# Performance work log

Hardware: AMD Instinct MI355X
Metric: run time of the kernel (lower is better)

The kernel has to match this reference:

```python
import jax, jax.numpy as jnp
import numpy as np

ALPHA = 0.3          # triplet margin
LOSS_WEIGHT = 1.0
VALID_COST = 100.0   # chosen so all queries are valid (query2gt ~ U[0,1))
POS_T = 3            # pos_thresh
NEG_T = 30           # neg_thresh
EPS = 1e-6           # torch pairwise_distance eps


def setup_inputs() -> dict:
    key0 = jax.random.key(0)
    ks = jax.random.split(key0, 6)
    Nq, V, K, D, G = 2048, 6, 4096, 256, 64
    attn = jax.random.normal(ks[0], (Nq, V, K), dtype=jnp.float32)
    query2gt = jax.random.uniform(ks[1], (Nq, G), dtype=jnp.float32)  # min < VALID_COST always
    query = jax.random.normal(ks[2], (Nq, V, D), dtype=jnp.float32)
    key = jax.random.normal(ks[3], (K, V, D), dtype=jnp.float32)
    pos_idx = jax.random.randint(ks[4], (V * Nq,), 0, POS_T, dtype=jnp.int64 if jax.config.jax_enable_x64 else jnp.int32)
    neg_idx = jax.random.randint(ks[5], (V * Nq,), POS_T, NEG_T, dtype=jnp.int64 if jax.config.jax_enable_x64 else jnp.int32)
    return {"attn": attn, "query2gt": query2gt, "query": query, "key": key,
            "pos_idx": pos_idx, "neg_idx": neg_idx}


def reference(attn, query2gt, query, key, pos_idx, neg_idx):
    # valid filtering: query2gt.min(-1) < VALID_COST is all-True by construction,
    # so no rows are dropped (keeps shapes static under jit).
    q = jnp.transpose(query, (1, 0, 2))   # [V, Nq, D]
    k = jnp.transpose(key, (1, 0, 2))     # [V, K, D]
    a = jnp.transpose(attn, (1, 0, 2))    # [V, Nq, K]
    V, Nq, K = a.shape

    # batched euclidean cdist per view via gram expansion
    qq = jnp.sum(q * q, axis=-1)[:, :, None]          # [V, Nq, 1]
    kk = jnp.sum(k * k, axis=-1)[:, None, :]          # [V, 1, K]
    d2 = qq + kk - 2.0 * jnp.einsum('vnd,vkd->vnk', q, k)
    dist = jnp.sqrt(jnp.maximum(d2, 0.0))             # [V, Nq, K]

    sorted_idx = jnp.argsort(dist, axis=-1).reshape(V * Nq, K)
    a = a.reshape(V * Nq, K)
    r = jnp.arange(V * Nq)

    pos = jax.nn.sigmoid(a[r, sorted_idx[r, pos_idx]])  # [V*Nq]
    neg = jax.nn.sigmoid(a[r, sorted_idx[r, neg_idx]])  # [V*Nq]

    # TripletMarginLoss(margin=ALPHA, p=1) with anchor = ones, 1-d embeddings
    d_pos = jnp.abs(1.0 - pos + EPS)
    d_neg = jnp.abs(1.0 - neg + EPS)
    loss = jnp.mean(jnp.maximum(d_pos - d_neg + ALPHA, 0.0))
    return LOSS_WEIGHT * loss
```

## Files before the change

kernel.cpp:

```cpp
#include <hip/hip_runtime.h>
#include <stdint.h>

#define NQ    2048
#define VV    6
#define KCNT  4096
#define DD    256
#define NROWS (VV*NQ)
#define ALPHA_M 0.3f
#define EPSL  1e-6f
#define SBIAS 256.0f
#define ZTHR  2.05f
#define CAP   256
#define NCHUNK 64
#define SLOTS  16

#define TM 128
#define TN 128
#define BKK 32

typedef _Float16 f16x8 __attribute__((ext_vector_type(8)));
typedef _Float16 f16x4 __attribute__((ext_vector_type(4)));
typedef float    f32x4 __attribute__((ext_vector_type(4)));

__device__ __forceinline__ void gload16(const void* g, void* l) {
    __builtin_amdgcn_global_load_lds(
        (__attribute__((address_space(1))) void*)(uintptr_t)g,
        (__attribute__((address_space(3))) void*)(uintptr_t)(uint32_t)(uintptr_t)l,
        16, 0, 0);
}

__device__ __forceinline__ unsigned ord16(_Float16 h) {
    unsigned short b = __builtin_bit_cast(unsigned short, h);
    return (b & 0x8000u) ? (unsigned)(~b & 0xFFFFu) : (unsigned)(b | 0x8000u);
}

__device__ __forceinline__ float triplet_term(const float* attn, int r, int kpos, int kneg) {
    int v = r / NQ, q = r - v * NQ;
    float apos = attn[(size_t)q * (VV*KCNT) + v*KCNT + kpos];
    float aneg = attn[(size_t)q * (VV*KCNT) + v*KCNT + kneg];
    float pv = 1.0f / (1.0f + expf(-apos));
    float nv = 1.0f / (1.0f + expf(-aneg));
    float dp = fabsf(1.0f - pv + EPSL);
    float dn = fabsf(1.0f - nv + EPSL);
    return fmaxf(dp - dn + ALPHA_M, 0.0f);
}

__global__ __launch_bounds__(256) void pack_fused(const float* __restrict__ key,
                                                  const float* __restrict__ query,
                                                  _Float16* __restrict__ Bpack,
                                                  _Float16* __restrict__ Apack,
                                                  float* __restrict__ kkp,
                                                  float* __restrict__ Trow,
                                                  unsigned* __restrict__ fcount,
                                                  float* __restrict__ out)
{
    int wid  = threadIdx.x >> 6;
    int lane = threadIdx.x & 63;
    if (blockIdx.x < 6144) {
        int rowid = blockIdx.x * 4 + wid;
        int k = rowid / 6;
        int v = rowid - k * 6;
        float4 x = *(const float4*)(key + (size_t)rowid * DD + lane * 4);
        f16x4 h;
        h.x = (_Float16)x.x; h.y = (_Float16)x.y;
        h.z = (_Float16)x.z; h.w = (_Float16)x.w;
        *(f16x4*)(Bpack + ((size_t)(v * KCNT + k)) * DD + lane * 4) = h;

        float s = x.x*x.x + x.y*x.y + x.z*x.z + x.w*x.w;
        #pragma unroll
        for (int off = 32; off >= 1; off >>= 1) s += __shfl_xor(s, off);
        if (lane == 0) kkp[v * KCNT + k] = s;
    } else {
        int bid2 = blockIdx.x - 6144;
        if (bid2 == 0) {
            if (threadIdx.x == 0) *fcount = 0;
            if (threadIdx.x == 1) out[0] = 0.0f;
        }
        int rowid = bid2 * 4 + wid;
        int q = rowid / 6;
        int v = rowid - q * 6;
        float4 x = *(const float4*)(query + (size_t)rowid * DD + lane * 4);
        f16x4 h;
        h.x = (_Float16)x.x; h.y = (_Float16)x.y;
        h.z = (_Float16)x.z; h.w = (_Float16)x.w;
        *(f16x4*)(Apack + ((size_t)(v * NQ + q)) * DD + lane * 4) = h;

        float qq = x.x*x.x + x.y*x.y + x.z*x.z + x.w*x.w;
        #pragma unroll
        for (int off = 32; off >= 1; off >>= 1) qq += __shfl_xor(qq, off);
        if (lane == 0)
            Trow[v * NQ + q] = 256.0f - ZTHR * sqrtf(512.0f + 4.0f * qq);
    }
}

__global__ __launch_bounds__(256) void score_gemm(const _Float16* __restrict__ Apack,
                                                  const _Float16* __restrict__ Bpack,
                                                  const float* __restrict__ kkp,
                                                  const float* __restrict__ Trow,
                                                  unsigned* __restrict__ cnt2,
                                                  unsigned* __restrict__ cand)
{
    __shared__ _Float16 As[TM * BKK];
    __shared__ _Float16 Bs[TN * BKK];

    int tid  = threadIdx.x;
    int wid  = tid >> 6;
    int lane = tid & 63;
    int c0   = blockIdx.x * TN;
    int grow = blockIdx.y * TM;
    int v    = grow / NQ;
    int q0   = grow - v * NQ;

    int srow = (wid << 4) + (lane >> 2);
    int sseg = (lane & 3) ^ ((lane >> 2) & 3);
    const _Float16* Ag0 = Apack + ((size_t)(v*NQ   + q0 + srow)) * DD + sseg*8;
    const _Float16* Ag1 = Ag0 + (size_t)64 * DD;
    const _Float16* Bg0 = Bpack + ((size_t)(v*KCNT + c0 + srow)) * DD + sseg*8;
    const _Float16* Bg1 = Bg0 + (size_t)64 * DD;

    _Float16* lA0 = As + wid*512;
    _Float16* lA1 = As + 2048 + wid*512;
    _Float16* lB0 = Bs + wid*512;
    _Float16* lB1 = Bs + 2048 + wid*512;

    int fr = lane & 15;
    int kg = lane >> 4;
    int rb = (wid >> 1) * 64;
    int cb = (wid & 1) * 64;
    int rg = lane >> 4;
    int ksw = (kg ^ (fr & 3)) << 3;

    f32x4 acc[4][4] = {};

    for (int kb = 0; kb < DD; kb += BKK) {
        __syncthreads();
        gload16(Ag0 + kb, lA0);
        gload16(Ag1 + kb, lA1);
        gload16(Bg0 + kb, lB0);
        gload16(Bg1 + kb, lB1);
        __syncthreads();

        f16x8 af[4], bf[4];
        #pragma unroll
        for (int m = 0; m < 4; ++m)
            af[m] = *(const f16x8*)&As[(rb + m*16 + fr)*BKK + ksw];
        #pragma unroll
        for (int n = 0; n < 4; ++n)
            bf[n] = *(const f16x8*)&Bs[(cb + n*16 + fr)*BKK + ksw];
        #pragma unroll
        for (int m = 0; m < 4; ++m)
            #pragma unroll
            for (int n = 0; n < 4; ++n)
                acc[m][n] = __builtin_amdgcn_mfma_f32_16x16x32_f16(af[m], bf[n], acc[m][n], 0, 0, 0);
    }

    int chunk = blockIdx.x * 2 + (wid & 1);
    float kkv[4];
    #pragma unroll
    for (int n = 0; n < 4; ++n)
        kkv[n] = kkp[v*KCNT + c0 + cb + n*16 + fr];

    unsigned ltm = (1u << fr) - 1u;
    int sh = rg * 16;

    #pragma unroll
    for (int m = 0; m < 4; ++m) {
        #pragma unroll
        for (int j = 0; j < 4; ++j) {
            int gr = grow + rb + m*16 + rg*4 + j;
            float Tr = Trow[gr];
            float s[4];
            unsigned g16[4];
            #pragma unroll
            for (int n = 0; n < 4; ++n) {
                s[n] = kkv[n] - 2.0f * acc[m][n][j];
                unsigned long long bal = __ballot(s[n] < Tr);
                g16[n] = (unsigned)(bal >> sh) & 0xFFFFu;
            }
            unsigned rank = 0;
            #pragma unroll
            for (int n = 0; n < 4; ++n) {
                if (s[n] < Tr) {
                    unsigned pos = rank + __popc(g16[n] & ltm);
                    if (pos < SLOTS)
                        cand[((size_t)gr << 10) + (chunk << 4) + pos] =
                            (ord16((_Float16)(s[n] - SBIAS)) << 12)
                            | (unsigned)(c0 + cb + n*16 + fr);
                }
                rank += __popc(g16[n]);
            }
            if (fr == 0) cnt2[(gr << 6) + chunk] = rank;
        }
    }
}

__global__ __launch_bounds__(256) void select2_kernel(const unsigned* __restrict__ cnt2,
                                                      const unsigned* __restrict__ cand,
                                                      const float* __restrict__ attn,
                                                      const int* __restrict__ pos_idx,
                                                      const int* __restrict__ neg_idx,
                                                      unsigned* __restrict__ fcount,
                                                      int* __restrict__ flist,
                                                      float* __restrict__ out)
{
    __shared__ unsigned cbuf[4][CAP];
    __shared__ float bsum;
    if (threadIdx.x == 0) bsum = 0.0f;
    __syncthreads();

    int wid  = threadIdx.x >> 6;
    int lane = threadIdx.x & 63;
    int r    = blockIdx.x * 4 + wid;
    int p = pos_idx[r];
    int n = neg_idx[r];

    unsigned c_l = cnt2[(r << 6) + lane];
    unsigned pre = c_l;
    #pragma unroll
    for (int off = 1; off <= 32; off <<= 1) {
        unsigned o = __shfl_up(pre, off);
        if (lane >= off) pre += o;
    }
    unsigned total = __shfl(pre, 63);
    unsigned excl  = pre - c_l;
    bool overflow  = __any(c_l > SLOTS);

    if (overflow || total < (unsigned)(n + 1) || total > CAP) {
        if (lane == 0) {
            unsigned i = atomicAdd(fcount, 1u);
            flist[i] = r;
        }
    } else {
        unsigned* mybuf = cbuf[wid];
        const unsigned* src = cand + ((size_t)r << 10) + (lane << 4);
        for (unsigned i = 0; i < c_l; ++i) mybuf[excl + i] = src[i];
        __asm__ volatile("s_waitcnt lgkmcnt(0)" ::: "memory");

        unsigned v0 = (lane       < (int)total) ? mybuf[lane]       : 0xFFFFFFFFu;
        unsigned v1 = (lane + 64  < (int)total) ? mybuf[lane + 64]  : 0xFFFFFFFFu;
        unsigned v2 = (lane + 128 < (int)total) ? mybuf[lane + 128] : 0xFFFFFFFFu;
        unsigned v3 = (lane + 192 < (int)total) ? mybuf[lane + 192] : 0xFFFFFFFFu;
        int kpos = 0, kneg = 0;
        for (int t = 0; t <= n; ++t) {
            unsigned m01 = v0 < v1 ? v0 : v1;
            unsigned m23 = v2 < v3 ? v2 : v3;
            unsigned m = m01 < m23 ? m01 : m23;
            #pragma unroll
            for (int off = 32; off >= 1; off >>= 1) {
                unsigned o = __shfl_xor(m, off);
                m = o < m ? o : m;
            }
            if      (v0 == m) v0 = 0xFFFFFFFFu;
            else if (v1 == m) v1 = 0xFFFFFFFFu;
            else if (v2 == m) v2 = 0xFFFFFFFFu;
            else if (v3 == m) v3 = 0xFFFFFFFFu;
            if (t == p) kpos = (int)(m & 0xFFFu);
            if (t == n) kneg = (int)(m & 0xFFFu);
        }
        if (lane == 0)
            atomicAdd(&bsum, triplet_term(attn, r, kpos, kneg) * (1.0f / (float)NROWS));
    }
    __syncthreads();
    if (threadIdx.x == 0) atomicAdd(out, bsum);
}

__global__ __launch_bounds__(256) void fallback_kernel(const _Float16* __restrict__ Apack,
                                                       const _Float16* __restrict__ Bpack,
                                                       const float* __restrict__ kkp,
                                                       const float* __restrict__ attn,
                                                       const int* __restrict__ pos_idx,
                                                       const int* __restrict__ neg_idx,
                                                       const unsigned* __restrict__ fcount,
                                                       const int* __restrict__ flist,
                                                       float* __restrict__ out)
{
    __shared__ float qrow[DD];
    __shared__ unsigned keys[KCNT];
    int nf = (int)*fcount;
    for (int it = blockIdx.x; it < nf; it += gridDim.x) {
        int r = flist[it];
        int v = r / NQ, q = r - v * NQ;
        qrow[threadIdx.x] = (float)Apack[((size_t)(v*NQ + q)) * DD + threadIdx.x];
        __syncthreads();
        for (int i = 0; i < 16; ++i) {
            int c = i * 256 + threadIdx.x;
            float dot = 0.0f;
            const f16x8* bp = (const f16x8*)(Bpack + ((size_t)(v*KCNT + c)) * DD);
            for (int d8 = 0; d8 < 32; ++d8) {
                f16x8 b = bp[d8];
                #pragma unroll
                for (int j = 0; j < 8; ++j) dot += qrow[d8*8 + j] * (float)b[j];
            }
            float s = kkp[v*KCNT + c] - 2.0f * dot;
            keys[c] = (ord16((_Float16)(s - SBIAS)) << 12) | (unsigned)c;
        }
        __syncthreads();
        if (threadIdx.x < 64) {
            int lane = threadIdx.x;
            int p = pos_idx[r], n = neg_idx[r];
            unsigned prev = 0;
            int kpos = 0, kneg = 0;
            for (int t = 0; t <= n; ++t) {
                unsigned m = 0xFFFFFFFFu;
                for (int i = 0; i < 64; ++i) {
                    unsigned kk2 = keys[i*64 + lane];
                    if (kk2 > prev && kk2 < m) m = kk2;
                }
                #pragma unroll
                for (int off = 32; off >= 1; off >>= 1) {
                    unsigned o = __shfl_xor(m, off);
                    m = o < m ? o : m;
                }
                if (t == p) kpos = (int)(m & 0xFFFu);
                if (t == n) kneg = (int)(m & 0xFFFu);
                prev = m;
            }
            if (lane == 0)
                atomicAdd(out, triplet_term(attn, r, kpos, kneg) * (1.0f / (float)NROWS));
        }
        __syncthreads();
    }
}

extern "C" void kernel_launch(void* const* d_in, const int* in_sizes, int n_in,
                              void* d_out, int out_size, void* d_ws, size_t ws_size,
                              hipStream_t stream)
{
    const float* attn    = (const float*)d_in[0];
    const float* query   = (const float*)d_in[2];
    const float* key     = (const float*)d_in[3];
    const int*   pos_idx = (const int*)d_in[4];
    const int*   neg_idx = (const int*)d_in[5];
    float* out = (float*)d_out;

    char* w = (char*)d_ws;
    unsigned* fcount   = (unsigned*)(w);
    float*    Trow     = (float*)   (w + 256);
    float*    kkp      = (float*)   (w + 49408);
    unsigned* cnt2     = (unsigned*)(w + 147712);
    int*      flist    = (int*)     (w + 3293440);
    _Float16* Apack    = (_Float16*)(w + 3342592);
    _Float16* Bpack    = (_Float16*)(w + 9634048);
    unsigned* cand     = (unsigned*)(w + 22216960);

    pack_fused<<<9216, 256, 0, stream>>>(key, query, Bpack, Apack, kkp, Trow,
                                         fcount, out);

    dim3 gg(KCNT / TN, NROWS / TM);
    score_gemm<<<gg, 256, 0, stream>>>(Apack, Bpack, kkp, Trow, cnt2, cand);

    select2_kernel<<<NROWS / 4, 256, 0, stream>>>(cnt2, cand, attn, pos_idx, neg_idx,
                                                  fcount, flist, out);
    fallback_kernel<<<64, 256, 0, stream>>>(Apack, Bpack, kkp, attn, pos_idx, neg_idx,
                                            fcount, flist, out);
}
```

Baseline: 129.4 us.

## Replace compacted candidate slots with per-chunk bitmasks and dense fp16 score matrix

The score GEMM no longer compacts threshold-passing candidates into fixed 16-slot buckets with counts. It now writes every score as fp16 into a dense row-major matrix, plus a 64-bit ballot mask per 64-column chunk. The select kernel popcounts the masks to build prefix offsets, then gathers the selected scores through the set bits. This removes the per-chunk slot-overflow fallback path and the rank computation in the GEMM epilogue, but adds a full fp16 write of the whole score matrix and scattered 2-byte gathers in the select kernel.

```diff
diff --git a/kernel.cpp b/kernel.cpp
--- a/kernel.cpp
+++ b/kernel.cpp
@@ -11,8 +11,6 @@
 #define SBIAS 256.0f
 #define ZTHR  2.05f
 #define CAP   256
-#define NCHUNK 64
-#define SLOTS  16
 
 #define TM 128
 #define TN 128
@@ -97,8 +95,8 @@
                                                   const _Float16* __restrict__ Bpack,
                                                   const float* __restrict__ kkp,
                                                   const float* __restrict__ Trow,
-                                                  unsigned* __restrict__ cnt2,
-                                                  unsigned* __restrict__ cand)
+                                                  unsigned long long* __restrict__ maskb,
+                                                  _Float16* __restrict__ wsf)
 {
     __shared__ _Float16 As[TM * BKK];
     __shared__ _Float16 Bs[TN * BKK];
@@ -160,7 +158,6 @@
     for (int n = 0; n < 4; ++n)
         kkv[n] = kkp[v*KCNT + c0 + cb + n*16 + fr];
 
-    unsigned ltm = (1u << fr) - 1u;
     int sh = rg * 16;
 
     #pragma unroll
@@ -169,33 +166,21 @@
         for (int j = 0; j < 4; ++j) {
             int gr = grow + rb + m*16 + rg*4 + j;
             float Tr = Trow[gr];
-            float s[4];
-            unsigned g16[4];
+            unsigned long long mk = 0;
             #pragma unroll
             for (int n = 0; n < 4; ++n) {
-                s[n] = kkv[n] - 2.0f * acc[m][n][j];
-                unsigned long long bal = __ballot(s[n] < Tr);
-                g16[n] = (unsigned)(bal >> sh) & 0xFFFFu;
+                float s = kkv[n] - 2.0f * acc[m][n][j];
+                wsf[(size_t)gr * KCNT + (c0 + cb + n*16 + fr)] = (_Float16)(s - SBIAS);
+                unsigned long long bal = __ballot(s < Tr);
+                mk |= (unsigned long long)((unsigned)(bal >> sh) & 0xFFFFu) << (n*16);
             }
-            unsigned rank = 0;
-            #pragma unroll
-            for (int n = 0; n < 4; ++n) {
-                if (s[n] < Tr) {
-                    unsigned pos = rank + __popc(g16[n] & ltm);
-                    if (pos < SLOTS)
-                        cand[((size_t)gr << 10) + (chunk << 4) + pos] =
-                            (ord16((_Float16)(s[n] - SBIAS)) << 12)
-                            | (unsigned)(c0 + cb + n*16 + fr);
-                }
-                rank += __popc(g16[n]);
-            }
-            if (fr == 0) cnt2[(gr << 6) + chunk] = rank;
-        }
-    }
-}
-
-__global__ __launch_bounds__(256) void select2_kernel(const unsigned* __restrict__ cnt2,
-                                                      const unsigned* __restrict__ cand,
+            if (fr == 0) maskb[((size_t)gr << 6) + chunk] = mk;
+        }
+    }
+}
+
+__global__ __launch_bounds__(256) void select2_kernel(const unsigned long long* __restrict__ maskb,
+                                                      const _Float16* __restrict__ wsf,
                                                       const float* __restrict__ attn,
                                                       const int* __restrict__ pos_idx,
                                                       const int* __restrict__ neg_idx,
@@ -214,7 +199,8 @@
     int p = pos_idx[r];
     int n = neg_idx[r];
 
-    unsigned c_l = cnt2[(r << 6) + lane];
+    unsigned long long mk = maskb[((size_t)r << 6) + lane];
+    unsigned c_l = (unsigned)__popcll(mk);
     unsigned pre = c_l;
     #pragma unroll
     for (int off = 1; off <= 32; off <<= 1) {
@@ -223,17 +209,23 @@
     }
     unsigned total = __shfl(pre, 63);
     unsigned excl  = pre - c_l;
-    bool overflow  = __any(c_l > SLOTS);
-
-    if (overflow || total < (unsigned)(n + 1) || total > CAP) {
+
+    if (total < (unsigned)(n + 1) || total > CAP) {
         if (lane == 0) {
             unsigned i = atomicAdd(fcount, 1u);
             flist[i] = r;
         }
     } else {
         unsigned* mybuf = cbuf[wid];
-        const unsigned* src = cand + ((size_t)r << 10) + (lane << 4);
-        for (unsigned i = 0; i < c_l; ++i) mybuf[excl + i] = src[i];
+        const _Float16* srow = wsf + (size_t)r * KCNT + (lane << 6);
+        unsigned idx = excl;
+        unsigned long long t = mk;
+        while (t) {
+            int b = __ffsll((long long)t) - 1;
+            t &= t - 1;
+            _Float16 h = srow[b];
+            mybuf[idx++] = (ord16(h) << 12) | (unsigned)((lane << 6) + b);
+        }
         __asm__ volatile("s_waitcnt lgkmcnt(0)" ::: "memory");
 
         unsigned v0 = (lane       < (int)total) ? mybuf[lane]       : 0xFFFFFFFFu;
@@ -241,7 +233,7 @@
         unsigned v2 = (lane + 128 < (int)total) ? mybuf[lane + 128] : 0xFFFFFFFFu;
         unsigned v3 = (lane + 192 < (int)total) ? mybuf[lane + 192] : 0xFFFFFFFFu;
         int kpos = 0, kneg = 0;
-        for (int t = 0; t <= n; ++t) {
+        for (int t2 = 0; t2 <= n; ++t2) {
             unsigned m01 = v0 < v1 ? v0 : v1;
             unsigned m23 = v2 < v3 ? v2 : v3;
             unsigned m = m01 < m23 ? m01 : m23;
@@ -254,8 +246,8 @@
             else if (v1 == m) v1 = 0xFFFFFFFFu;
             else if (v2 == m) v2 = 0xFFFFFFFFu;
             else if (v3 == m) v3 = 0xFFFFFFFFu;
-            if (t == p) kpos = (int)(m & 0xFFFu);
-            if (t == n) kneg = (int)(m & 0xFFFu);
+            if (t2 == p) kpos = (int)(m & 0xFFFu);
+            if (t2 == n) kneg = (int)(m & 0xFFFu);
         }
         if (lane == 0)
             atomicAdd(&bsum, triplet_term(attn, r, kpos, kneg) * (1.0f / (float)NROWS));
@@ -334,22 +326,22 @@
     float* out = (float*)d_out;
 
     char* w = (char*)d_ws;
-    unsigned* fcount   = (unsigned*)(w);
-    float*    Trow     = (float*)   (w + 256);
-    float*    kkp      = (float*)   (w + 49408);
-    unsigned* cnt2     = (unsigned*)(w + 147712);
-    int*      flist    = (int*)     (w + 3293440);
-    _Float16* Apack    = (_Float16*)(w + 3342592);
-    _Float16* Bpack    = (_Float16*)(w + 9634048);
-    unsigned* cand     = (unsigned*)(w + 22216960);
+    unsigned*           fcount = (unsigned*)(w);
+    float*              Trow   = (float*)   (w + 256);
+    float*              kkp    = (float*)   (w + 49408);
+    int*                flist  = (int*)     (w + 147712);
+    unsigned long long* maskb  = (unsigned long long*)(w + 196864);
+    _Float16*           Apack  = (_Float16*)(w + 6488320);
+    _Float16*           Bpack  = (_Float16*)(w + 12779776);
+    _Float16*           wsf    = (_Float16*)(w + 25362688);
 
     pack_fused<<<9216, 256, 0, stream>>>(key, query, Bpack, Apack, kkp, Trow,
                                          fcount, out);
 
     dim3 gg(KCNT / TN, NROWS / TM);
-    score_gemm<<<gg, 256, 0, stream>>>(Apack, Bpack, kkp, Trow, cnt2, cand);
-
-    select2_kernel<<<NROWS / 4, 256, 0, stream>>>(cnt2, cand, attn, pos_idx, neg_idx,
+    score_gemm<<<gg, 256, 0, stream>>>(Apack, Bpack, kkp, Trow, maskb, wsf);
+
+    select2_kernel<<<NROWS / 4, 256, 0, stream>>>(maskb, wsf, attn, pos_idx, neg_idx,
                                                   fcount, flist, out);
     fallback_kernel<<<64, 256, 0, stream>>>(Apack, Bpack, kkp, attn, pos_idx, neg_idx,
                                             fcount, flist, out);
```

Measured after the change: 125.1 us. 1.03x faster.
